# Kernel optimization log

Hardware: AMD Instinct MI355X
Metric: run time of the kernel (lower is better)

The kernel has to match this reference:

```python
import jax, jax.numpy as jnp
import numpy as np

EPS = 1e-5

def _layernorm(x, g, b):
    mu = jnp.mean(x, axis=-1, keepdims=True)
    var = jnp.mean(jnp.square(x - mu), axis=-1, keepdims=True)
    return (x - mu) * jax.lax.rsqrt(var + EPS) * g + b

def setup_inputs() -> dict:
    key = jax.random.key(0)
    ks = jax.random.split(key, 4)
    E, B, D, H = 8, 131072, 128, 128
    features = jax.random.normal(ks[0], (E, B, D), dtype=jnp.float32)
    gate_w1 = jax.random.normal(ks[1], (E * D, H), dtype=jnp.float32) * (1.0 / np.sqrt(E * D))
    gate_b1 = jnp.zeros((H,), dtype=jnp.float32)
    ln1_g = jnp.ones((H,), dtype=jnp.float32)
    ln1_b = jnp.zeros((H,), dtype=jnp.float32)
    gate_w2 = jax.random.normal(ks[2], (H, E), dtype=jnp.float32) * (1.0 / np.sqrt(H))
    gate_b2 = jnp.zeros((E,), dtype=jnp.float32)
    out_g = jnp.ones((D,), dtype=jnp.float32)
    out_b = jnp.zeros((D,), dtype=jnp.float32)
    return {"features": features, "gate_w1": gate_w1, "gate_b1": gate_b1,
            "ln1_g": ln1_g, "ln1_b": ln1_b, "gate_w2": gate_w2, "gate_b2": gate_b2,
            "out_g": out_g, "out_b": out_b}

def reference(features, gate_w1, gate_b1, ln1_g, ln1_b, gate_w2, gate_b2, out_g, out_b):
    # features: [E, B, D]
    E, B, D = features.shape
    # concat teacher features per sample -> [B, E*D]
    concat = jnp.transpose(features, (1, 0, 2)).reshape(B, E * D)
    h = concat @ gate_w1 + gate_b1                       # [B, 128]
    h = jax.nn.gelu(h, approximate=False)                # torch nn.GELU default = exact
    h = _layernorm(h, ln1_g, ln1_b)
    logits = h @ gate_w2 + gate_b2                       # [B, E]
    scores = jax.nn.softmax(logits, axis=-1)             # [B, E]
    # per-expert scalar weight then LayerNorm over D
    weighted = scores.T[:, :, None] * features           # [E, B, D]
    out = _layernorm(weighted, out_g, out_b)             # [E, B, D]
    return out
```

## Files before the change

kernel.cpp:

```cpp
#include <hip/hip_runtime.h>
#include <hip/hip_bf16.h>

#define B_N   131072
#define E_N   8
#define D_N   128
#define H_N   128
#define K_N   1024
#define MBLK  16
#define NTHR  256

typedef __attribute__((ext_vector_type(8))) short bf16x8;
typedef __attribute__((ext_vector_type(4))) float f32x4;
typedef __attribute__((ext_vector_type(4))) unsigned short u16x4;

__device__ __forceinline__ unsigned short f2bf(float f) {
    union { float f; unsigned int i; } c; c.f = f;
    unsigned int x = c.i;
    return (unsigned short)((x + 0x7fffu + ((x >> 16) & 1u)) >> 16);
}
__device__ __forceinline__ float bf2f(unsigned short u) {
    union { unsigned int i; float f; } c; c.i = ((unsigned int)u) << 16; return c.f;
}

__global__ void prep_w1_frags(const float* __restrict__ w1,
                              unsigned short* __restrict__ frag) {
    int t    = blockIdx.x * blockDim.x + threadIdx.x;
    int lane = t & 63;
    int fgi  = t >> 6;
    int kst  = fgi >> 3;
    int nt   = fgi & 7;
    int n    = nt * 16 + (lane & 15);
    int k0   = kst * 32 + (lane >> 4) * 8;
    bf16x8 v;
    #pragma unroll
    for (int j = 0; j < 8; ++j)
        v[j] = (short)f2bf(w1[(k0 + j) * H_N + n]);
    *reinterpret_cast<bf16x8*>(frag + (size_t)t * 8) = v;
}

__global__ __launch_bounds__(NTHR, 3)
void moe_fused(const float* __restrict__ feats,
               const unsigned short* __restrict__ w1frag,
               const float* __restrict__ gate_b1,
               const float* __restrict__ ln1_g,
               const float* __restrict__ ln1_b,
               const float* __restrict__ gate_w2,
               const float* __restrict__ gate_b2,
               const float* __restrict__ out_g,
               const float* __restrict__ out_b,
               float* __restrict__ out)
{
    __shared__ __attribute__((aligned(16))) unsigned short featS[MBLK * K_N];
    __shared__ float hS[MBLK * 132];
    __shared__ float w2tS[E_N * H_N];
    __shared__ float gb1S[H_N], l1gS[H_N], l1bS[H_N], ogS[D_N], obS[D_N];
    __shared__ float gb2S[E_N];
    __shared__ float scoreS[MBLK * E_N];

    const int tid = threadIdx.x;
    const int b0  = blockIdx.x * MBLK;

    if (tid < 128) {
        gb1S[tid] = gate_b1[tid];
        l1gS[tid] = ln1_g[tid];
        l1bS[tid] = ln1_b[tid];
        ogS[tid]  = out_g[tid];
        obS[tid]  = out_b[tid];
    }
    if (tid < 8) gb2S[tid] = gate_b2[tid];
    for (int idx = tid; idx < H_N * E_N; idx += NTHR)
        w2tS[(idx & 7) * H_N + (idx >> 3)] = gate_w2[idx];

    #pragma unroll
    for (int e = 0; e < E_N; ++e) {
        const f32x4* src = reinterpret_cast<const f32x4*>(
            feats + ((size_t)e * B_N + b0) * D_N);
        #pragma unroll
        for (int i = 0; i < (MBLK * D_N / 4) / NTHR; ++i) {
            int f   = tid + i * NTHR;
            f32x4 v = src[f];
            int m   = f >> 5;
            int dq  = f & 31;
            int k   = e * D_N + dq * 4;
            int uoff = m * K_N + ((((k >> 3) ^ (m & 7)) << 3) | (k & 7));
            u16x4 u;
            u[0] = f2bf(v[0]); u[1] = f2bf(v[1]);
            u[2] = f2bf(v[2]); u[3] = f2bf(v[3]);
            *reinterpret_cast<u16x4*>(&featS[uoff]) = u;
        }
    }
    __syncthreads();

    const int wv   = tid >> 6;
    const int lane = tid & 63;
    const int lrow = lane & 15;
    const int lkh  = lane >> 4;
    const int nt0  = wv * 2, nt1 = nt0 + 1;
    f32x4 acc0 = {0.f, 0.f, 0.f, 0.f};
    f32x4 acc1 = {0.f, 0.f, 0.f, 0.f};
    const bf16x8* wf = reinterpret_cast<const bf16x8*>(w1frag);
    const int arow = lrow * K_N;
    const int asw  = lrow & 7;
    #pragma unroll 4
    for (int kk = 0; kk < 32; ++kk) {
        bf16x8 a  = *reinterpret_cast<const bf16x8*>(
            &featS[arow + ((((kk << 2) + lkh) ^ asw) << 3)]);
        bf16x8 b0 = wf[((kk * 8 + nt0) << 6) + lane];
        bf16x8 b1 = wf[((kk * 8 + nt1) << 6) + lane];
        acc0 = __builtin_amdgcn_mfma_f32_16x16x32_bf16(a, b0, acc0, 0, 0, 0);
        acc1 = __builtin_amdgcn_mfma_f32_16x16x32_bf16(a, b1, acc1, 0, 0, 0);
    }

    {
        const int colA = nt0 * 16 + lrow;
        const int colB = nt1 * 16 + lrow;
        #pragma unroll
        for (int r = 0; r < 4; ++r) {
            int row  = lkh * 4 + r;
            float vA = acc0[r] + gb1S[colA];
            float vB = acc1[r] + gb1S[colB];
            vA = 0.5f * vA * (1.f + erff(vA * 0.70710678118654752f));
            vB = 0.5f * vB * (1.f + erff(vB * 0.70710678118654752f));
            hS[row * 132 + colA] = vA;
            hS[row * 132 + colB] = vB;
        }
    }
    __syncthreads();

    {
        const int row = tid >> 4;
        const int gl  = tid & 15;
        const float* hrow = &hS[row * 132 + gl * 8];
        float hv[8];
        #pragma unroll
        for (int j = 0; j < 8; ++j) hv[j] = hrow[j];
        float s = 0.f, sq = 0.f;
        #pragma unroll
        for (int j = 0; j < 8; ++j) { s += hv[j]; sq += hv[j] * hv[j]; }
        #pragma unroll
        for (int msk = 1; msk < 16; msk <<= 1) {
            s  += __shfl_xor(s, msk);
            sq += __shfl_xor(sq, msk);
        }
        float mu  = s * (1.f / 128.f);
        float var = sq * (1.f / 128.f) - mu * mu;
        float rs  = rsqrtf(var + 1e-5f);
        float p[8] = {0.f, 0.f, 0.f, 0.f, 0.f, 0.f, 0.f, 0.f};
        #pragma unroll
        for (int j = 0; j < 8; ++j) {
            int col  = gl * 8 + j;
            float hn = (hv[j] - mu) * rs * l1gS[col] + l1bS[col];
            #pragma unroll
            for (int e = 0; e < 8; ++e) p[e] += hn * w2tS[e * H_N + col];
        }
        #pragma unroll
        for (int msk = 1; msk < 16; msk <<= 1) {
            #pragma unroll
            for (int e = 0; e < 8; ++e) p[e] += __shfl_xor(p[e], msk);
        }
        float lg[8], mx = -3.0e38f;
        #pragma unroll
        for (int e = 0; e < 8; ++e) { lg[e] = p[e] + gb2S[e]; mx = fmaxf(mx, lg[e]); }
        float den = 0.f, ex[8];
        #pragma unroll
        for (int e = 0; e < 8; ++e) { ex[e] = __expf(lg[e] - mx); den += ex[e]; }
        float inv = 1.f / den;
        if (gl < 8) scoreS[row * 8 + gl] = ex[gl] * inv;
    }
    __syncthreads();

    {
        const int m  = tid >> 4;
        const int gl = tid & 15;
        #pragma unroll
        for (int e = 0; e < E_N; ++e) {
            int slot = ((e << 4) | gl) ^ (m & 7);
            bf16x8 x8 = *reinterpret_cast<const bf16x8*>(&featS[m * K_N + (slot << 3)]);
            float x[8];
            #pragma unroll
            for (int j = 0; j < 8; ++j) x[j] = bf2f((unsigned short)x8[j]);
            float s = 0.f, sq = 0.f;
            #pragma unroll
            for (int j = 0; j < 8; ++j) { s += x[j]; sq += x[j] * x[j]; }
            #pragma unroll
            for (int msk = 1; msk < 16; msk <<= 1) {
                s  += __shfl_xor(s, msk);
                sq += __shfl_xor(sq, msk);
            }
            float mu  = s * (1.f / 128.f);
            float var = sq * (1.f / 128.f) - mu * mu;
            float sc  = scoreS[m * 8 + e];
            float srs = sc * rsqrtf(sc * sc * var + 1e-5f);
            float* dst = out + ((size_t)e * B_N + b0 + m) * D_N + gl * 8;
            f32x4 o0, o1;
            #pragma unroll
            for (int j = 0; j < 4; ++j)
                o0[j] = (x[j] - mu) * srs * ogS[gl * 8 + j] + obS[gl * 8 + j];
            #pragma unroll
            for (int j = 0; j < 4; ++j)
                o1[j] = (x[4 + j] - mu) * srs * ogS[gl * 8 + 4 + j] + obS[gl * 8 + 4 + j];
            *reinterpret_cast<f32x4*>(dst)     = o0;
            *reinterpret_cast<f32x4*>(dst + 4) = o1;
        }
    }
}

extern "C" void kernel_launch(void* const* d_in, const int* in_sizes, int n_in,
                              void* d_out, int out_size, void* d_ws, size_t ws_size,
                              hipStream_t stream) {
    const float* feats   = (const float*)d_in[0];
    const float* gate_w1 = (const float*)d_in[1];
    const float* gate_b1 = (const float*)d_in[2];
    const float* ln1_g   = (const float*)d_in[3];
    const float* ln1_b   = (const float*)d_in[4];
    const float* gate_w2 = (const float*)d_in[5];
    const float* gate_b2 = (const float*)d_in[6];
    const float* out_g   = (const float*)d_in[7];
    const float* out_b   = (const float*)d_in[8];
    float* outp = (float*)d_out;
    unsigned short* frag = (unsigned short*)d_ws;

    prep_w1_frags<<<64, NTHR, 0, stream>>>(gate_w1, frag);
    moe_fused<<<B_N / MBLK, NTHR, 0, stream>>>(
        feats, frag, gate_b1, ln1_g, ln1_b, gate_w2, gate_b2, out_g, out_b, outp);
}
```

Baseline: 301.5 us.

## Shrink LDS footprint: drop staged params, store hidden in bf16, raise occupancy

Measured after the change: 308.4 us. 2.3% more time.

```diff
diff --git a/kernel.cpp b/kernel.cpp
--- a/kernel.cpp
+++ b/kernel.cpp
@@ -38,7 +38,7 @@
     *reinterpret_cast<bf16x8*>(frag + (size_t)t * 8) = v;
 }
 
-__global__ __launch_bounds__(NTHR, 3)
+__global__ __launch_bounds__(NTHR, 4)
 void moe_fused(const float* __restrict__ feats,
                const unsigned short* __restrict__ w1frag,
                const float* __restrict__ gate_b1,
@@ -51,25 +51,11 @@
                float* __restrict__ out)
 {
     __shared__ __attribute__((aligned(16))) unsigned short featS[MBLK * K_N];
-    __shared__ float hS[MBLK * 132];
-    __shared__ float w2tS[E_N * H_N];
-    __shared__ float gb1S[H_N], l1gS[H_N], l1bS[H_N], ogS[D_N], obS[D_N];
-    __shared__ float gb2S[E_N];
+    __shared__ __attribute__((aligned(16))) unsigned short hSb[MBLK * 136];
     __shared__ float scoreS[MBLK * E_N];
 
     const int tid = threadIdx.x;
     const int b0  = blockIdx.x * MBLK;
-
-    if (tid < 128) {
-        gb1S[tid] = gate_b1[tid];
-        l1gS[tid] = ln1_g[tid];
-        l1bS[tid] = ln1_b[tid];
-        ogS[tid]  = out_g[tid];
-        obS[tid]  = out_b[tid];
-    }
-    if (tid < 8) gb2S[tid] = gate_b2[tid];
-    for (int idx = tid; idx < H_N * E_N; idx += NTHR)
-        w2tS[(idx & 7) * H_N + (idx >> 3)] = gate_w2[idx];
 
     #pragma unroll
     for (int e = 0; e < E_N; ++e) {
@@ -114,15 +100,17 @@
     {
         const int colA = nt0 * 16 + lrow;
         const int colB = nt1 * 16 + lrow;
+        const float bA = gate_b1[colA];
+        const float bB = gate_b1[colB];
         #pragma unroll
         for (int r = 0; r < 4; ++r) {
             int row  = lkh * 4 + r;
-            float vA = acc0[r] + gb1S[colA];
-            float vB = acc1[r] + gb1S[colB];
+            float vA = acc0[r] + bA;
+            float vB = acc1[r] + bB;
             vA = 0.5f * vA * (1.f + erff(vA * 0.70710678118654752f));
             vB = 0.5f * vB * (1.f + erff(vB * 0.70710678118654752f));
-            hS[row * 132 + colA] = vA;
-            hS[row * 132 + colB] = vB;
+            hSb[row * 136 + colA] = f2bf(vA);
+            hSb[row * 136 + colB] = f2bf(vB);
         }
     }
     __syncthreads();
@@ -130,10 +118,10 @@
     {
         const int row = tid >> 4;
         const int gl  = tid & 15;
-        const float* hrow = &hS[row * 132 + gl * 8];
+        bf16x8 h8 = *reinterpret_cast<const bf16x8*>(&hSb[row * 136 + gl * 8]);
         float hv[8];
         #pragma unroll
-        for (int j = 0; j < 8; ++j) hv[j] = hrow[j];
+        for (int j = 0; j < 8; ++j) hv[j] = bf2f((unsigned short)h8[j]);
         float s = 0.f, sq = 0.f;
         #pragma unroll
         for (int j = 0; j < 8; ++j) { s += hv[j]; sq += hv[j] * hv[j]; }
@@ -145,13 +133,23 @@
         float mu  = s * (1.f / 128.f);
         float var = sq * (1.f / 128.f) - mu * mu;
         float rs  = rsqrtf(var + 1e-5f);
+        const f32x4* lgv = reinterpret_cast<const f32x4*>(ln1_g + gl * 8);
+        const f32x4* lbv = reinterpret_cast<const f32x4*>(ln1_b + gl * 8);
+        f32x4 lg0 = lgv[0], lg1 = lgv[1];
+        f32x4 lb0 = lbv[0], lb1 = lbv[1];
         float p[8] = {0.f, 0.f, 0.f, 0.f, 0.f, 0.f, 0.f, 0.f};
         #pragma unroll
         for (int j = 0; j < 8; ++j) {
             int col  = gl * 8 + j;
-            float hn = (hv[j] - mu) * rs * l1gS[col] + l1bS[col];
-            #pragma unroll
-            for (int e = 0; e < 8; ++e) p[e] += hn * w2tS[e * H_N + col];
+            float g  = (j < 4) ? lg0[j & 3] : lg1[j & 3];
+            float bb = (j < 4) ? lb0[j & 3] : lb1[j & 3];
+            float hn = (hv[j] - mu) * rs * g + bb;
+            const f32x4* w2v = reinterpret_cast<const f32x4*>(gate_w2 + col * 8);
+            f32x4 wa = w2v[0], wb = w2v[1];
+            #pragma unroll
+            for (int e = 0; e < 4; ++e) p[e]     += hn * wa[e];
+            #pragma unroll
+            for (int e = 0; e < 4; ++e) p[e + 4] += hn * wb[e];
         }
         #pragma unroll
         for (int msk = 1; msk < 16; msk <<= 1) {
@@ -160,7 +158,7 @@
         }
         float lg[8], mx = -3.0e38f;
         #pragma unroll
-        for (int e = 0; e < 8; ++e) { lg[e] = p[e] + gb2S[e]; mx = fmaxf(mx, lg[e]); }
+        for (int e = 0; e < 8; ++e) { lg[e] = p[e] + gate_b2[e]; mx = fmaxf(mx, lg[e]); }
         float den = 0.f, ex[8];
         #pragma unroll
         for (int e = 0; e < 8; ++e) { ex[e] = __expf(lg[e] - mx); den += ex[e]; }
@@ -172,6 +170,10 @@
     {
         const int m  = tid >> 4;
         const int gl = tid & 15;
+        const f32x4* ogv = reinterpret_cast<const f32x4*>(out_g + gl * 8);
+        const f32x4* obv = reinterpret_cast<const f32x4*>(out_b + gl * 8);
+        f32x4 og0 = ogv[0], og1 = ogv[1];
+        f32x4 ob0 = obv[0], ob1 = obv[1];
         #pragma unroll
         for (int e = 0; e < E_N; ++e) {
             int slot = ((e << 4) | gl) ^ (m & 7);
@@ -195,10 +197,10 @@
             f32x4 o0, o1;
             #pragma unroll
             for (int j = 0; j < 4; ++j)
-                o0[j] = (x[j] - mu) * srs * ogS[gl * 8 + j] + obS[gl * 8 + j];
+                o0[j] = (x[j] - mu) * srs * og0[j] + ob0[j];
             #pragma unroll
             for (int j = 0; j < 4; ++j)
-                o1[j] = (x[4 + j] - mu) * srs * ogS[gl * 8 + 4 + j] + obS[gl * 8 + 4 + j];
+                o1[j] = (x[4 + j] - mu) * srs * og1[j] + ob1[j];
             *reinterpret_cast<f32x4*>(dst)     = o0;
             *reinterpret_cast<f32x4*>(dst + 4) = o1;
         }
```
